# Optimization experiments

Measured on AMD Instinct MI355X. Metric: run time of the kernel, lower is better.

The kernel has to match this reference:

```python
import jax, jax.numpy as jnp
import numpy as np

H = 16  # head_count


def _split_heads(x, h):
    b, l, d = x.shape
    return x.reshape(b, l, h, d // h).transpose(0, 2, 1, 3)  # [B,H,L,d/H]


def setup_inputs() -> dict:
    key = jax.random.key(0)
    ks = jax.random.split(key, 12)
    B, Lk, Dk, Dq, Dm = 32, 2048, 1024, 1024, 1024
    d = Dm // H
    U = 0.08  # torch init uniform_(-0.08, 0.08)
    inp = {
        "key": jax.random.normal(ks[0], (B, Lk, Dk), jnp.float32),
        "value": jax.random.normal(ks[1], (B, Lk, Dk), jnp.float32),
        "query": jax.random.normal(ks[2], (B, 1, Dq), jnp.float32),
        "mask": jax.random.randint(ks[3], (B, Lk), 0, 2).astype(bool).at[:, 0].set(False),
        "Wk": jax.random.uniform(ks[4], (Dk, Dm), jnp.float32, -U, U),
        "bk": jax.random.uniform(ks[5], (Dm,), jnp.float32, -U, U),
        "Wq": jax.random.uniform(ks[6], (Dq, Dm), jnp.float32, -U, U),
        "bq": jax.random.uniform(ks[7], (Dm,), jnp.float32, -U, U),
        "w_score": jax.random.uniform(ks[8], (d,), jnp.float32, -U, U),
        "b_score": jax.random.uniform(ks[9], (1,), jnp.float32, -U, U),
        "Wf": jax.random.uniform(ks[10], (Dk, Dk), jnp.float32, -U, U),
        "bf": jax.random.uniform(ks[11], (Dk,), jnp.float32, -U, U),
    }
    return inp


def reference(key, value, query, mask, Wk, bk, Wq, bq, w_score, b_score, Wf, bf):
    B = key.shape[0]
    key_up = _split_heads(key @ Wk + bk, H)      # [B,H,Lk,d]
    value_up = _split_heads(value, H)            # [B,H,Lk,dv]
    query_up = _split_heads(query @ Wq + bq, H)  # [B,H,1,d]
    # additive attention: tanh(q+k) . w  -> scalar score per key position
    scores = jnp.einsum('bhld,d->bhl', jnp.tanh(query_up + key_up), w_score) + b_score[0]
    scores = jnp.where(mask[:, None, :], -jnp.inf, scores)
    attn = jax.nn.softmax(scores, axis=-1)       # [B,H,Lk]
    context = jnp.einsum('bhl,bhld->bhd', attn, value_up)  # [B,H,dv]
    context = context.reshape(B, 1, -1)          # combine heads -> [B,1,Dk]
    output = context @ Wf + bf
    return output, attn[:, :, None, :]
```

## Files before the change

### kernel.cpp

```cpp
#include <hip/hip_runtime.h>
#include <hip/hip_bf16.h>

#define B_  32
#define LK  2048
#define DM  1024
#define NH  16

typedef __attribute__((ext_vector_type(8))) short short8;
typedef __attribute__((ext_vector_type(4))) float f32x4;

__device__ __forceinline__ ushort f2bf(float f){
  union { float f; unsigned u; } v; v.f = f;
  unsigned u = v.u;
  u += 0x7fffu + ((u >> 16) & 1u);
  return (ushort)(u >> 16);
}

__device__ __forceinline__ short8 pack8(f32x4 a, f32x4 b){
  union { __hip_bfloat162 h[4]; short8 s; } r;
  r.h[0] = __float22bfloat162_rn(make_float2(a[0], a[1]));
  r.h[1] = __float22bfloat162_rn(make_float2(a[2], a[3]));
  r.h[2] = __float22bfloat162_rn(make_float2(b[0], b[1]));
  r.h[3] = __float22bfloat162_rn(make_float2(b[2], b[3]));
  return r.s;
}

__device__ __forceinline__ void gll16(const void* g, void* l){
  __builtin_amdgcn_global_load_lds(
      (__attribute__((address_space(1))) void*)g,
      (__attribute__((address_space(3))) void*)l, 16, 0, 0);
}

#define C2LOG2E 2.8853900817779268f

__global__ __launch_bounds__(256) void k_pre(const float* __restrict__ Wk, ushort* __restrict__ wkt,
                                             const float* __restrict__ query, const float* __restrict__ Wq,
                                             const float* __restrict__ bq, float* __restrict__ qup){
  __shared__ float smem[1056];
  int bid = blockIdx.x;
  int t = threadIdx.x;
  if (bid < 1024){
    float (*tile)[33] = (float(*)[33])smem;
    int n0 = (bid & 31) * 32, k0 = (bid >> 5) * 32;
    int tx = t & 31, ty = t >> 5;
#pragma unroll
    for (int r = 0; r < 4; ++r)
      tile[ty + 8*r][tx] = Wk[(size_t)(k0 + ty + 8*r) * DM + n0 + tx];
    __syncthreads();
#pragma unroll
    for (int r = 0; r < 4; ++r){
      int n = ty + 8*r;
      wkt[(size_t)(n0 + n) * DM + k0 + tx] = f2bf(tile[tx][n]);
    }
  } else {
    int bb = bid - 1024;
    int b = bb >> 2, nc = bb & 3;
    float* q = smem;
#pragma unroll
    for (int j = 0; j < 4; ++j) q[j*256 + t] = query[(size_t)b*DM + j*256 + t];
    __syncthreads();
    int n = nc*256 + t;
    float acc = bq[n];
#pragma unroll 16
    for (int k = 0; k < DM; ++k) acc += q[k] * Wq[(size_t)k*DM + n];
    qup[(size_t)b*DM + n] = acc;
  }
}

__global__ __launch_bounds__(256, 2) void k_gemm(
    const float* __restrict__ key, const ushort* __restrict__ wkt,
    const float* __restrict__ qup, const float* __restrict__ bk,
    const float* __restrict__ wsc, float* __restrict__ scores)
{
  __shared__ ushort ldsA[128*64];
  __shared__ ushort ldsB0[256*64];
  __shared__ ushort ldsB1[256*64];
  const int tid  = threadIdx.x;
  const int lane = tid & 63;
  const int wc   = tid >> 6;
  const int l15  = lane & 15, l16 = lane >> 4;

  const int bid = blockIdx.x;
  const int xcd = bid & 7;
  const int j   = bid >> 3;
  const int ct4 = j & 3;
  const int rb  = xcd * 64 + (j >> 2);
  const size_t row0 = (size_t)rb * 128;
  const int b  = rb >> 4;
  const int l0 = (rb & 15) * 128;

  const int rlo = tid >> 3;
  const int g8  = rlo & 7;
  const int sk8 = (tid & 7) ^ g8;
  const float*  akey  = key + (row0 + (size_t)rlo) * DM + sk8*8;
  const ushort* bbase = wkt + ((size_t)ct4*256 + rlo) * DM + sk8*8;

  float qbc[4], wm2[4], wsum = 0.f;
#pragma unroll
  for (int ni = 0; ni < 4; ++ni){
    int n = ct4*256 + wc*64 + ni*16 + l15;
    float w = wsc[ni*16 + l15];
    qbc[ni] = (qup[(size_t)b*DM + n] + bk[n]) * C2LOG2E;
    wm2[ni] = -2.f * w;
    wsum   += w;
  }

  f32x4 acc[8][4];
#pragma unroll
  for (int mi = 0; mi < 8; ++mi)
#pragma unroll
    for (int ni = 0; ni < 4; ++ni) acc[mi][ni] = (f32x4){0.f,0.f,0.f,0.f};

  const int sw = (l15 & 7) << 4;

  short8 sa[4];
#pragma unroll
  for (int c = 0; c < 4; ++c){
    const float* ap = akey + (size_t)c*32*DM;
    f32x4 x0 = *(const f32x4*)ap, x1 = *(const f32x4*)(ap + 4);
    sa[c] = pack8(x0, x1);
  }
#pragma unroll
  for (int c = 0; c < 8; ++c)
    gll16(bbase + (size_t)c*32*DM, (char*)ldsB0 + (c*256 + tid)*16);

  for (int kt = 0; kt < 16; ++kt){
#pragma unroll
    for (int c = 0; c < 4; ++c)
      *(short8*)((char*)ldsA + (c*256 + tid)*16) = sa[c];
    asm volatile("s_waitcnt vmcnt(0) lgkmcnt(0)" ::: "memory");
    __builtin_amdgcn_s_barrier();
    asm volatile("" ::: "memory");

    const char* Bc = (const char*)((kt & 1) ? ldsB1 : ldsB0);
    char*       Bn = (char*)((kt & 1) ? ldsB0 : ldsB1);
    f32x4 a0[4], a1[4];
    if (kt < 15){
#pragma unroll
      for (int c = 0; c < 8; ++c)
        gll16(bbase + (size_t)(kt+1)*64 + (size_t)c*32*DM, Bn + (c*256 + tid)*16);
#pragma unroll
      for (int c = 0; c < 4; ++c){
        const float* ap = akey + (size_t)c*32*DM + (kt+1)*64;
        a0[c] = *(const f32x4*)ap; a1[c] = *(const f32x4*)(ap + 4);
      }
    }

#pragma unroll
    for (int kk = 0; kk < 2; ++kk){
      short8 af[8], bfr[4];
#pragma unroll
      for (int mi = 0; mi < 8; ++mi){
        int row = mi*16 + l15;
        af[mi] = *(const short8*)((const char*)ldsA + row*128 + ((kk*64 + l16*16) ^ sw));
      }
#pragma unroll
      for (int ni = 0; ni < 4; ++ni){
        int col = wc*64 + ni*16 + l15;
        bfr[ni] = *(const short8*)(Bc + col*128 + ((kk*64 + l16*16) ^ sw));
      }
      __builtin_amdgcn_s_setprio(1);
#pragma unroll
      for (int mi = 0; mi < 8; ++mi)
#pragma unroll
        for (int ni = 0; ni < 4; ++ni)
          acc[mi][ni] = __builtin_amdgcn_mfma_f32_16x16x32_bf16(af[mi], bfr[ni], acc[mi][ni], 0, 0, 0);
      __builtin_amdgcn_s_setprio(0);
    }

    if (kt < 15){
#pragma unroll
      for (int c = 0; c < 4; ++c)
        sa[c] = pack8(a0[c], a1[c]);
    }
    __builtin_amdgcn_s_barrier();
    asm volatile("" ::: "memory");
  }

#pragma unroll
  for (int mi = 0; mi < 8; ++mi){
    f32x4 s = {wsum, wsum, wsum, wsum};
#pragma unroll
    for (int ni = 0; ni < 4; ++ni)
#pragma unroll
      for (int r = 0; r < 4; ++r){
        float a  = fmaf(acc[mi][ni][r], C2LOG2E, qbc[ni]);
        float e  = __builtin_amdgcn_exp2f(a);
        float rc = __builtin_amdgcn_rcpf(e + 1.f);
        s[r] = fmaf(wm2[ni], rc, s[r]);
      }
#pragma unroll
    for (int r = 0; r < 4; ++r){
      float v = s[r];
      v += __shfl_xor(v, 1);
      v += __shfl_xor(v, 2);
      v += __shfl_xor(v, 4);
      v += __shfl_xor(v, 8);
      s[r] = v;
    }
    if (l15 == 0)
      *(f32x4*)(scores + (size_t)(b*NH + ct4*4 + wc)*LK + l0 + mi*16 + l16*4) = s;
  }
}

__global__ __launch_bounds__(256) void k_smctx(const float* __restrict__ scr, const int* __restrict__ mask,
                                               const float* __restrict__ value, float* __restrict__ attn,
                                               float* __restrict__ ctxbuf){
  __shared__ float red[8];
  __shared__ float sm[LK];
  const int bh = blockIdx.x;
  const int b = bh >> 4, h = bh & 15;
  const float* s = scr + (size_t)bh * LK;
  const int*   m = mask + (size_t)b * LK;
  float*       a = attn + (size_t)bh * LK;
  const int t = threadIdx.x;

  float sv[8]; int mv[8];
  float lmax = -1e30f;
#pragma unroll
  for (int j = 0; j < 8; ++j){
    int i = j*256 + t;
    sv[j] = s[i]; mv[j] = m[i];
    if (!mv[j]) lmax = fmaxf(lmax, sv[j]);
  }
#pragma unroll
  for (int off = 32; off >= 1; off >>= 1) lmax = fmaxf(lmax, __shfl_xor(lmax, off));
  if ((t & 63) == 0) red[t >> 6] = lmax;
  __syncthreads();
  lmax = fmaxf(fmaxf(red[0], red[1]), fmaxf(red[2], red[3]));

  float ev[8]; float lsum = 0.f;
#pragma unroll
  for (int j = 0; j < 8; ++j){
    ev[j] = mv[j] ? 0.f : __expf(sv[j] - lmax);
    lsum += ev[j];
  }
#pragma unroll
  for (int off = 32; off >= 1; off >>= 1) lsum += __shfl_xor(lsum, off);
  if ((t & 63) == 0) red[4 + (t >> 6)] = lsum;
  __syncthreads();
  lsum = red[4] + red[5] + red[6] + red[7];
  float inv = 1.f / lsum;
#pragma unroll
  for (int j = 0; j < 8; ++j){
    float w = ev[j] * inv;
    a[j*256 + t]  = w;
    sm[j*256 + t] = w;
  }
  __syncthreads();

  const int c2 = (t & 31) * 2, w = t >> 5;
  const float* vp = value + ((size_t)b*LK + (size_t)w*256)*DM + h*64 + c2;
  const float* smw = sm + w*256;
  float px = 0.f, py = 0.f, qx = 0.f, qy = 0.f;
#pragma unroll 2
  for (int l = 0; l < 256; l += 2){
    float2 v0 = *(const float2*)(vp + (size_t)l*DM);
    float2 v1 = *(const float2*)(vp + (size_t)(l+1)*DM);
    px = fmaf(smw[l],   v0.x, px); py = fmaf(smw[l],   v0.y, py);
    qx = fmaf(smw[l+1], v1.x, qx); qy = fmaf(smw[l+1], v1.y, qy);
  }
  float2 tot = make_float2(px + qx, py + qy);
  __syncthreads();
  *(float2*)&sm[w*64 + c2] = tot;
  __syncthreads();
  if (t < 64){
    float r = 0.f;
#pragma unroll
    for (int g = 0; g < 8; ++g) r += sm[g*64 + t];
    ctxbuf[(size_t)b*DM + h*64 + t] = r;
  }
}

__global__ __launch_bounds__(256) void k_out(const float* __restrict__ ctxbuf, const float* __restrict__ Wf,
                                             const float* __restrict__ bfv, float* __restrict__ out){
  __shared__ float ctx[DM];
  int b = blockIdx.x >> 2, nc = blockIdx.x & 3;
  int t = threadIdx.x;
#pragma unroll
  for (int j = 0; j < 4; ++j)
    ctx[j*256 + t] = ctxbuf[(size_t)b*DM + j*256 + t];
  __syncthreads();
  int n = nc*256 + t;
  float acc = bfv[n];
#pragma unroll 16
  for (int k = 0; k < DM; ++k) acc += ctx[k] * Wf[(size_t)k*DM + n];
  out[(size_t)b*DM + n] = acc;
}

extern "C" void kernel_launch(void* const* d_in, const int* in_sizes, int n_in,
                              void* d_out, int out_size, void* d_ws, size_t ws_size,
                              hipStream_t stream){
  (void)in_sizes; (void)n_in; (void)out_size; (void)ws_size;
  const float* key   = (const float*)d_in[0];
  const float* value = (const float*)d_in[1];
  const float* query = (const float*)d_in[2];
  const int*   mask  = (const int*)d_in[3];
  const float* Wk    = (const float*)d_in[4];
  const float* bk    = (const float*)d_in[5];
  const float* Wq    = (const float*)d_in[6];
  const float* bq    = (const float*)d_in[7];
  const float* wsc   = (const float*)d_in[8];
  const float* Wf    = (const float*)d_in[10];
  const float* bfv   = (const float*)d_in[11];

  float* out0 = (float*)d_out;
  float* attn = out0 + (size_t)B_ * DM;

  char* ws = (char*)d_ws;
  ushort* wkt  = (ushort*)(ws);
  float*  qup  = (float*)(ws + (2u<<20));
  float*  scr  = (float*)(ws + (2u<<20) + (128u<<10));
  float*  ctxb = (float*)(ws + (2u<<20) + (128u<<10) + (4u<<20));

  k_pre<<<1152, 256, 0, stream>>>(Wk, wkt, query, Wq, bq, qup);
  k_gemm<<<2048, 256, 0, stream>>>(key, wkt, qup, bk, wsc, scr);
  k_smctx<<<512, 256, 0, stream>>>(scr, mask, value, attn, ctxb);
  k_out<<<128, 256, 0, stream>>>(ctxb, Wf, bfv, out0);
}
```

Before: 290.5 us.

## Compact unmasked key rows and skip GEMM panels for masked positions

Extra k_pre blocks run a prefix-sum compaction of unmasked key indices per batch, padded to 128-row panels, and store a count per batch. k_gemm gathers key rows through the index list and exits early for panels beyond the unmasked count. Scores are scatter-written only for kept positions. The aim is to avoid the projection GEMM and tanh work for masked keys, about half of them, at the cost of indirect row loads and a small scan pre-pass.

```diff
diff --git a/kernel.cpp b/kernel.cpp
--- a/kernel.cpp
+++ b/kernel.cpp
@@ -35,11 +35,40 @@
 
 __global__ __launch_bounds__(256) void k_pre(const float* __restrict__ Wk, ushort* __restrict__ wkt,
                                              const float* __restrict__ query, const float* __restrict__ Wq,
-                                             const float* __restrict__ bq, float* __restrict__ qup){
+                                             const float* __restrict__ bq, float* __restrict__ qup,
+                                             const int* __restrict__ mask, int* __restrict__ idxv,
+                                             int* __restrict__ cntv){
   __shared__ float smem[1056];
   int bid = blockIdx.x;
   int t = threadIdx.x;
-  if (bid < 1024){
+  if (bid >= 1152){
+    int bb = bid - 1152;
+    const int* m = mask + (size_t)bb * LK;
+    int* idxb = idxv + (size_t)bb * LK;
+    int* ps = (int*)smem;
+    int keep[8]; int c8 = 0;
+#pragma unroll
+    for (int u = 0; u < 8; ++u){
+      keep[u] = (m[t*8 + u] == 0);
+      c8 += keep[u];
+    }
+    ps[t] = c8; __syncthreads();
+    for (int off = 1; off < 256; off <<= 1){
+      int v = (t >= off) ? ps[t - off] : 0;
+      __syncthreads();
+      ps[t] += v;
+      __syncthreads();
+    }
+    int pos = ps[t] - c8;
+    int tot = ps[255];
+#pragma unroll
+    for (int u = 0; u < 8; ++u){
+      if (keep[u]) idxb[pos++] = t*8 + u;
+    }
+    int pad = ((tot + 127) >> 7) << 7;
+    for (int p = tot + t; p < pad; p += 256) idxb[p] = 0;
+    if (t == 0) cntv[bb] = tot;
+  } else if (bid < 1024){
     float (*tile)[33] = (float(*)[33])smem;
     int n0 = (bid & 31) * 32, k0 = (bid >> 5) * 32;
     int tx = t & 31, ty = t >> 5;
@@ -70,7 +99,8 @@
 __global__ __launch_bounds__(256, 2) void k_gemm(
     const float* __restrict__ key, const ushort* __restrict__ wkt,
     const float* __restrict__ qup, const float* __restrict__ bk,
-    const float* __restrict__ wsc, float* __restrict__ scores)
+    const float* __restrict__ wsc, float* __restrict__ scores,
+    const int* __restrict__ idxv, const int* __restrict__ cntv)
 {
   __shared__ ushort ldsA[128*64];
   __shared__ ushort ldsB0[256*64];
@@ -85,15 +115,24 @@
   const int j   = bid >> 3;
   const int ct4 = j & 3;
   const int rb  = xcd * 64 + (j >> 2);
-  const size_t row0 = (size_t)rb * 128;
-  const int b  = rb >> 4;
-  const int l0 = (rb & 15) * 128;
+  const int b     = rb >> 4;
+  const int panel = rb & 15;
+
+  const int cnt = cntv[b];
+  if (panel * 128 >= cnt) return;
+  const int* idxb = idxv + (size_t)b * LK;
 
   const int rlo = tid >> 3;
   const int g8  = rlo & 7;
   const int sk8 = (tid & 7) ^ g8;
-  const float*  akey  = key + (row0 + (size_t)rlo) * DM + sk8*8;
   const ushort* bbase = wkt + ((size_t)ct4*256 + rlo) * DM + sk8*8;
+
+  const float* akey[4];
+#pragma unroll
+  for (int c = 0; c < 4; ++c){
+    int rowc = panel*128 + rlo + c*32;
+    akey[c] = key + ((size_t)b * LK + idxb[rowc]) * DM + sk8*8;
+  }
 
   float qbc[4], wm2[4], wsum = 0.f;
 #pragma unroll
@@ -116,7 +155,7 @@
   short8 sa[4];
 #pragma unroll
   for (int c = 0; c < 4; ++c){
-    const float* ap = akey + (size_t)c*32*DM;
+    const float* ap = akey[c];
     f32x4 x0 = *(const f32x4*)ap, x1 = *(const f32x4*)(ap + 4);
     sa[c] = pack8(x0, x1);
   }
@@ -141,7 +180,7 @@
         gll16(bbase + (size_t)(kt+1)*64 + (size_t)c*32*DM, Bn + (c*256 + tid)*16);
 #pragma unroll
       for (int c = 0; c < 4; ++c){
-        const float* ap = akey + (size_t)c*32*DM + (kt+1)*64;
+        const float* ap = akey[c] + (kt+1)*64;
         a0[c] = *(const f32x4*)ap; a1[c] = *(const f32x4*)(ap + 4);
       }
     }
@@ -177,6 +216,7 @@
     asm volatile("" ::: "memory");
   }
 
+  const size_t srow = (size_t)(b*NH + ct4*4 + wc) * LK;
 #pragma unroll
   for (int mi = 0; mi < 8; ++mi){
     f32x4 s = {wsum, wsum, wsum, wsum};
@@ -198,8 +238,14 @@
       v += __shfl_xor(v, 8);
       s[r] = v;
     }
-    if (l15 == 0)
-      *(f32x4*)(scores + (size_t)(b*NH + ct4*4 + wc)*LK + l0 + mi*16 + l16*4) = s;
+    if (l15 == 0){
+      int rowc0 = panel*128 + mi*16 + l16*4;
+#pragma unroll
+      for (int r = 0; r < 4; ++r){
+        int rowc = rowc0 + r;
+        if (rowc < cnt) scores[srow + idxb[rowc]] = s[r];
+      }
+    }
   }
 }
 
@@ -312,9 +358,11 @@
   float*  qup  = (float*)(ws + (2u<<20));
   float*  scr  = (float*)(ws + (2u<<20) + (128u<<10));
   float*  ctxb = (float*)(ws + (2u<<20) + (128u<<10) + (4u<<20));
-
-  k_pre<<<1152, 256, 0, stream>>>(Wk, wkt, query, Wq, bq, qup);
-  k_gemm<<<2048, 256, 0, stream>>>(key, wkt, qup, bk, wsc, scr);
+  int*    idxv = (int*)  (ws + (2u<<20) + (256u<<10) + (4u<<20));
+  int*    cntv = (int*)  (ws + (2u<<20) + (512u<<10) + (4u<<20));
+
+  k_pre<<<1184, 256, 0, stream>>>(Wk, wkt, query, Wq, bq, qup, mask, idxv, cntv);
+  k_gemm<<<2048, 256, 0, stream>>>(key, wkt, qup, bk, wsc, scr, idxv, cntv);
   k_smctx<<<512, 256, 0, stream>>>(scr, mask, value, attn, ctxb);
   k_out<<<128, 256, 0, stream>>>(ctxb, Wf, bfv, out0);
 }
```

After: 249.7 us. 14.1% less time.
